# Kernel optimization log

Measured on AMD Instinct MI355X. Metric: run time of the kernel, lower is better.

## Reference

```python
import jax, jax.numpy as jnp
import numpy as np

SCALE_WEIGHT = 0.5 ** 0.5
B, C, T, S = 8, 512, 2048, 2048


def setup_inputs() -> dict:
    key = jax.random.key(0)
    ks = jax.random.split(key, 6)
    return {
        "base_target_emb": jax.random.normal(ks[0], (B, C, T, 1), dtype=jnp.float32),
        "input_from_dec": jax.random.normal(ks[1], (B, C, T, 1), dtype=jnp.float32),
        "encoder_out_top": jax.random.normal(ks[2], (B, C, S), dtype=jnp.float32),
        "encoder_out_combine": jax.random.normal(ks[3], (B, C, S), dtype=jnp.float32),
        "W": jax.random.normal(ks[4], (C, C), dtype=jnp.float32) * (1.0 / np.sqrt(C)),
        "b": jax.random.normal(ks[5], (C,), dtype=jnp.float32) * 0.01,
    }


def reference(base_target_emb, input_from_dec, encoder_out_top, encoder_out_combine, W, b):
    # seq_linear: per-token Linear over the channel dim. torch Linear: h = x @ W.T + b, W is [out,in]
    x = input_from_dec[..., 0]                                # [B,C,T]
    preatt = jnp.einsum('oc,bct->bot', W, x) + b[None, :, None]  # [B,C,T]
    target = (base_target_emb[..., 0] + preatt) * SCALE_WEIGHT   # [B,C,T]
    pre_attn = jnp.einsum('bct,bcs->bts', target, encoder_out_top)  # [B,T,S]
    attn = jax.nn.softmax(pre_attn, axis=2)                      # [B,T,S]
    ctx = jnp.einsum('bts,bcs->btc', attn, encoder_out_combine)  # [B,T,C]
    context_output = jnp.transpose(ctx, (0, 2, 1))[..., None]    # [B,C,T,1]
    return context_output, attn
```

## Files before the change

### kernel.cpp

```cpp
#include <hip/hip_runtime.h>
#include <cstddef>
#include <cstdint>

#define SCALE_WEIGHT 0.70710678118654752440f

static constexpr int B_ = 8, C_ = 512, T_ = 2048, S_ = 2048;
static constexpr size_t BCT_ = (size_t)B_ * C_ * T_;
static constexpr size_t BTS_ = (size_t)B_ * T_ * S_;

typedef _Float16 half_t;
typedef half_t half8  __attribute__((ext_vector_type(8)));
typedef half_t half4v __attribute__((ext_vector_type(4)));
typedef float  floatx4 __attribute__((ext_vector_type(4)));

__device__ __forceinline__ void gload_lds16(const void* g, void* l) {
    __builtin_amdgcn_global_load_lds(
        (const __attribute__((address_space(1))) void*)g,
        (__attribute__((address_space(3))) void*)l, 16, 0, 0);
}

__global__ __launch_bounds__(256) void transpose_cvt_kernel(
    const float* __restrict__ in, half_t* __restrict__ out, int R, int Cc)
{
    __shared__ float tile[64][65];
    const int b  = blockIdx.z;
    const int r0 = blockIdx.y * 64, c0 = blockIdx.x * 64;
    const float* ib = in + (size_t)b * R * Cc;
    half_t* ob = out + (size_t)b * R * Cc;
    const int t  = threadIdx.x;
    const int rr = t >> 4, cq = t & 15;
    #pragma unroll
    for (int i = 0; i < 4; ++i) {
        const int r = rr + i * 16;
        float4 v = *(const float4*)&ib[(size_t)(r0 + r) * Cc + c0 + cq * 4];
        tile[cq * 4 + 0][r] = v.x;
        tile[cq * 4 + 1][r] = v.y;
        tile[cq * 4 + 2][r] = v.z;
        tile[cq * 4 + 3][r] = v.w;
    }
    __syncthreads();
    const int cw = t >> 4, rq = (t & 15) * 4;
    #pragma unroll
    for (int i = 0; i < 4; ++i) {
        const int c = cw + i * 16;
        half4v h = {(half_t)tile[c][rq + 0], (half_t)tile[c][rq + 1],
                    (half_t)tile[c][rq + 2], (half_t)tile[c][rq + 3]};
        *(half4v*)&ob[(size_t)(c0 + c) * R + r0 + rq] = h;
    }
}

__global__ __launch_bounds__(256) void cvt_f32_f16_kernel(
    const float* __restrict__ in, half_t* __restrict__ out, int n4)
{
    const int stride = gridDim.x * blockDim.x;
    for (int i = blockIdx.x * blockDim.x + threadIdx.x; i < n4; i += stride) {
        float4 v = ((const float4*)in)[i];
        half4v h = {(half_t)v.x, (half_t)v.y, (half_t)v.z, (half_t)v.w};
        ((half4v*)out)[i] = h;
    }
}

template<int EPI>
__global__ __launch_bounds__(256) void gemm_f16_db_kernel(
    const half_t* __restrict__ A, const half_t* __restrict__ Bm,
    float* __restrict__ Cout, half_t* __restrict__ CoutH,
    const float* __restrict__ base, const float* __restrict__ bias,
    int M, int N, int K, size_t sA, size_t sB, size_t sC)
{
    __shared__ __align__(128) half_t As[2][128 * 64];
    __shared__ __align__(128) half_t Bs[2][128 * 64];

    const int tid  = threadIdx.x;
    const int lane = tid & 63, w = tid >> 6;
    const int wr = w >> 1, wc = w & 1;
    const int b  = blockIdx.z;
    const int m0 = blockIdx.y * 128, n0 = blockIdx.x * 128;

    const half_t* Ab = A  + (size_t)b * sA;
    const half_t* Bb = Bm + (size_t)b * sB;

    const int lr = lane >> 3;
    const int sw = (lane & 7) ^ lr;
    const half_t* aG[4]; const half_t* bG[4];
    int dOff[4];
    #pragma unroll
    for (int i = 0; i < 4; ++i) {
        const int r = w * 32 + i * 8 + lr;
        aG[i] = Ab + (size_t)(m0 + r) * K + sw * 8;
        bG[i] = Bb + (size_t)(n0 + r) * K + sw * 8;
        dOff[i] = (w * 32 + i * 8) * 128;
    }

    const int fr = lane & 15, kg = lane >> 4;
    int aoff[4], boff[4];
    #pragma unroll
    for (int mi = 0; mi < 4; ++mi) {
        const int m = wr * 64 + mi * 16 + fr;
        aoff[mi] = m * 128 + ((kg ^ (m & 7)) << 4);
    }
    #pragma unroll
    for (int nj = 0; nj < 4; ++nj) {
        const int n = wc * 64 + nj * 16 + fr;
        boff[nj] = n * 128 + ((kg ^ (n & 7)) << 4);
    }

    floatx4 acc[4][4];
    #pragma unroll
    for (int mi = 0; mi < 4; ++mi)
        #pragma unroll
        for (int nj = 0; nj < 4; ++nj)
            acc[mi][nj] = (floatx4){0.f, 0.f, 0.f, 0.f};

    auto STAGE = [&](int t, int pg) {
        const int k0 = t * 64;
        char* Ad = (char*)As[pg];
        char* Bd = (char*)Bs[pg];
        #pragma unroll
        for (int i = 0; i < 4; ++i) {
            gload_lds16(aG[i] + k0, Ad + dOff[i]);
            gload_lds16(bG[i] + k0, Bd + dOff[i]);
        }
    };

    auto COMPUTE = [&](int pg) {
        const char* Ar = (const char*)As[pg];
        const char* Br = (const char*)Bs[pg];
        #pragma unroll
        for (int kk = 0; kk < 2; ++kk) {
            half8 af[4], bf[4];
            #pragma unroll
            for (int mi = 0; mi < 4; ++mi)
                af[mi] = *(const half8*)(Ar + (aoff[mi] ^ (kk << 6)));
            #pragma unroll
            for (int nj = 0; nj < 4; ++nj)
                bf[nj] = *(const half8*)(Br + (boff[nj] ^ (kk << 6)));
            #pragma unroll
            for (int mi = 0; mi < 4; ++mi)
                #pragma unroll
                for (int nj = 0; nj < 4; ++nj)
                    acc[mi][nj] = __builtin_amdgcn_mfma_f32_16x16x32_f16(
                        af[mi], bf[nj], acc[mi][nj], 0, 0, 0);
        }
    };

    const int NT = K >> 6;
    STAGE(0, 0);
    int cur = 0;
    for (int t = 0; t < NT - 1; ++t) {
        STAGE(t + 1, cur ^ 1);
        asm volatile("s_waitcnt vmcnt(8)" ::: "memory");
        __builtin_amdgcn_s_barrier();
        __builtin_amdgcn_sched_barrier(0);
        COMPUTE(cur);
        asm volatile("s_waitcnt lgkmcnt(0)" ::: "memory");
        __builtin_amdgcn_sched_barrier(0);
        __builtin_amdgcn_s_barrier();
        __builtin_amdgcn_sched_barrier(0);
        cur ^= 1;
    }
    asm volatile("s_waitcnt vmcnt(0)" ::: "memory");
    __builtin_amdgcn_s_barrier();
    __builtin_amdgcn_sched_barrier(0);
    COMPUTE(cur);

    if constexpr (EPI == 0) {
        float* Cb = Cout + (size_t)b * sC;
        #pragma unroll
        for (int mi = 0; mi < 4; ++mi) {
            const int row = m0 + wr * 64 + mi * 16 + (lane >> 4) * 4;
            #pragma unroll
            for (int nj = 0; nj < 4; ++nj) {
                const int col = n0 + wc * 64 + nj * 16 + (lane & 15);
                #pragma unroll
                for (int r = 0; r < 4; ++r)
                    Cb[(size_t)(row + r) * N + col] = acc[mi][nj][r];
            }
        }
    } else {
        half_t* Cb = CoutH + (size_t)b * sC;
        #pragma unroll
        for (int nj = 0; nj < 4; ++nj) {
            const int col = n0 + wc * 64 + nj * 16 + (lane & 15);
            const float bn = bias[col];
            const float* bp = base + ((size_t)b * N + col) * (size_t)M;
            #pragma unroll
            for (int mi = 0; mi < 4; ++mi) {
                const int row = m0 + wr * 64 + mi * 16 + (lane >> 4) * 4;
                #pragma unroll
                for (int r = 0; r < 4; ++r) {
                    float v = (acc[mi][nj][r] + bn + bp[row + r]) * SCALE_WEIGHT;
                    Cb[(size_t)(row + r) * N + col] = (half_t)v;
                }
            }
        }
    }
}

__global__ __launch_bounds__(256) void k3_softmax_kernel(
    float* __restrict__ logits, half_t* __restrict__ attnh)
{
    float* p = logits + (size_t)blockIdx.x * S_;
    half4v* ph = (half4v*)(attnh + (size_t)blockIdx.x * S_);
    const int tid = threadIdx.x;
    float4 v0 = *(const float4*)&p[tid * 4];
    float4 v1 = *(const float4*)&p[tid * 4 + 1024];

    float mx = fmaxf(fmaxf(fmaxf(v0.x, v0.y), fmaxf(v0.z, v0.w)),
                     fmaxf(fmaxf(v1.x, v1.y), fmaxf(v1.z, v1.w)));
    #pragma unroll
    for (int off = 32; off; off >>= 1)
        mx = fmaxf(mx, __shfl_xor(mx, off));

    __shared__ float sm[4];
    __shared__ float ss[4];
    const int wid = tid >> 6, lane = tid & 63;
    if (lane == 0) sm[wid] = mx;
    __syncthreads();
    const float rmax = fmaxf(fmaxf(sm[0], sm[1]), fmaxf(sm[2], sm[3]));

    float e[8];
    e[0] = __expf(v0.x - rmax); e[1] = __expf(v0.y - rmax);
    e[2] = __expf(v0.z - rmax); e[3] = __expf(v0.w - rmax);
    e[4] = __expf(v1.x - rmax); e[5] = __expf(v1.y - rmax);
    e[6] = __expf(v1.z - rmax); e[7] = __expf(v1.w - rmax);

    float sum = 0.f;
    #pragma unroll
    for (int i = 0; i < 8; ++i) sum += e[i];
    #pragma unroll
    for (int off = 32; off; off >>= 1)
        sum += __shfl_xor(sum, off);
    if (lane == 0) ss[wid] = sum;
    __syncthreads();
    const float inv = 1.f / (ss[0] + ss[1] + ss[2] + ss[3]);

    float4 r0, r1;
    r0.x = e[0] * inv; r0.y = e[1] * inv; r0.z = e[2] * inv; r0.w = e[3] * inv;
    r1.x = e[4] * inv; r1.y = e[5] * inv; r1.z = e[6] * inv; r1.w = e[7] * inv;
    *(float4*)&p[tid * 4] = r0;
    *(float4*)&p[tid * 4 + 1024] = r1;
    ph[tid]       = (half4v){(half_t)r0.x, (half_t)r0.y, (half_t)r0.z, (half_t)r0.w};
    ph[tid + 256] = (half4v){(half_t)r1.x, (half_t)r1.y, (half_t)r1.z, (half_t)r1.w};
}

extern "C" void kernel_launch(void* const* d_in, const int* in_sizes, int n_in,
                              void* d_out, int out_size, void* d_ws, size_t ws_size,
                              hipStream_t stream) {
    const float* base = (const float*)d_in[0];
    const float* x    = (const float*)d_in[1];
    const float* top  = (const float*)d_in[2];
    const float* comb = (const float*)d_in[3];
    const float* W    = (const float*)d_in[4];
    const float* bias = (const float*)d_in[5];

    float* out    = (float*)d_out;
    float* ctx    = out;
    float* logits = out + BCT_;

    half_t* xT   = (half_t*)d_out;
    half_t* topT = xT + BCT_;

    half_t* attnh = (half_t*)d_ws;
    half_t* tgtT  = attnh;
    half_t* combh = attnh + BTS_;
    half_t* Wh    = combh + (size_t)B_ * C_ * S_;

    transpose_cvt_kernel<<<dim3(T_ / 64, C_ / 64, B_), 256, 0, stream>>>(x, xT, C_, T_);
    transpose_cvt_kernel<<<dim3(S_ / 64, C_ / 64, B_), 256, 0, stream>>>(top, topT, C_, S_);
    cvt_f32_f16_kernel<<<2048, 256, 0, stream>>>(comb, combh, (int)((size_t)B_ * C_ * S_ / 4));
    cvt_f32_f16_kernel<<<256, 256, 0, stream>>>(W, Wh, C_ * C_ / 4);

    gemm_f16_db_kernel<1><<<dim3(C_ / 128, T_ / 128, B_), 256, 0, stream>>>(
        xT, Wh, nullptr, tgtT, base, bias,
        T_, C_, C_, (size_t)T_ * C_, 0, (size_t)T_ * C_);

    gemm_f16_db_kernel<0><<<dim3(S_ / 128, T_ / 128, B_), 256, 0, stream>>>(
        tgtT, topT, logits, nullptr, nullptr, nullptr,
        T_, S_, C_, (size_t)T_ * C_, (size_t)S_ * C_, (size_t)T_ * S_);

    k3_softmax_kernel<<<dim3(B_ * T_), 256, 0, stream>>>(logits, attnh);

    gemm_f16_db_kernel<0><<<dim3(T_ / 128, C_ / 128, B_), 256, 0, stream>>>(
        combh, attnh, ctx, nullptr, nullptr, nullptr,
        C_, T_, S_, (size_t)C_ * S_, (size_t)T_ * S_, (size_t)C_ * T_);
}
```

Baseline: 212.0 us.

## Fuse logits GEMM with online softmax into one kernel

Replaces the QK^T GEMM plus separate softmax kernel with a fused kernel. Each 512-thread block computes 64 rows across all of S, tracks an online running max and sum, and stores unnormalized fp16 exponentials to a workspace. It then rescales them into the fp32 attn output and the fp16 copy. This removes the fp32 logits write and re-read, at the cost of a 64-row tile per block and only 256 blocks, which may underuse the GPU, plus an extra fp16 workspace round trip.

```diff
diff --git a/kernel.cpp b/kernel.cpp
--- a/kernel.cpp
+++ b/kernel.cpp
@@ -196,51 +196,199 @@
     }
 }
 
-__global__ __launch_bounds__(256) void k3_softmax_kernel(
-    float* __restrict__ logits, half_t* __restrict__ attnh)
+__global__ __launch_bounds__(512) void k23_fused_kernel(
+    const half_t* __restrict__ tgtT, const half_t* __restrict__ topT,
+    float* __restrict__ attnf, half_t* __restrict__ attnh,
+    half_t* __restrict__ pws)
 {
-    float* p = logits + (size_t)blockIdx.x * S_;
-    half4v* ph = (half4v*)(attnh + (size_t)blockIdx.x * S_);
-    const int tid = threadIdx.x;
-    float4 v0 = *(const float4*)&p[tid * 4];
-    float4 v1 = *(const float4*)&p[tid * 4 + 1024];
-
-    float mx = fmaxf(fmaxf(fmaxf(v0.x, v0.y), fmaxf(v0.z, v0.w)),
-                     fmaxf(fmaxf(v1.x, v1.y), fmaxf(v1.z, v1.w)));
-    #pragma unroll
-    for (int off = 32; off; off >>= 1)
-        mx = fmaxf(mx, __shfl_xor(mx, off));
-
-    __shared__ float sm[4];
-    __shared__ float ss[4];
-    const int wid = tid >> 6, lane = tid & 63;
-    if (lane == 0) sm[wid] = mx;
+    __shared__ __align__(128) half_t Atile[64 * 512];
+    __shared__ __align__(128) half_t Bbuf[2][128 * 64];
+    __shared__ __align__(128) half_t ptile[64 * 128];
+    __shared__ float mu[16 * 64];
+    __shared__ float msh[64], ssh[64];
+    __shared__ float pmax[4][64], psum[4][64];
+
+    const int tid = threadIdx.x, lane = tid & 63, w = tid >> 6;
+    const int wr = w >> 2, wc = w & 3;
+    const int b = blockIdx.x, tt = blockIdx.y;
+    const int fr = lane & 15, kg = lane >> 4;
+    const int q4 = (lane >> 4) << 2;
+
+    const half_t* Ab = tgtT + ((size_t)(b * T_ + tt * 64)) * C_;
+    const half_t* Bb = topT + (size_t)b * S_ * C_;
+    half_t* pblk = pws + ((size_t)(b * 32 + tt)) * 64 * 2048;
+
+    if (tid < 64) { msh[tid] = -3.0e38f; ssh[tid] = 0.f; }
+
+    #pragma unroll
+    for (int i = 0; i < 8; ++i) {
+        const int row = w * 8 + i;
+        gload_lds16(Ab + (size_t)row * C_ + ((lane ^ (row & 7)) << 3),
+                    (char*)Atile + row * 1024);
+    }
+
+    auto STAGE_B = [&](int q, int pg) {
+        const int s0 = (q >> 3) * 128, k0 = (q & 7) * 64;
+        char* dst = (char*)Bbuf[pg];
+        #pragma unroll
+        for (int j = 0; j < 2; ++j) {
+            const int r8 = w * 16 + j * 8;
+            gload_lds16(Bb + (size_t)(s0 + r8 + (lane >> 3)) * C_ + k0 +
+                            (((lane & 7) ^ (lane >> 3)) << 3),
+                        dst + r8 * 128);
+        }
+    };
+
+    STAGE_B(0, 0);
+    int buf = 0;
+
+    for (int st = 0; st < 16; ++st) {
+        floatx4 acc[2][2];
+        #pragma unroll
+        for (int mi = 0; mi < 2; ++mi)
+            #pragma unroll
+            for (int nj = 0; nj < 2; ++nj)
+                acc[mi][nj] = (floatx4){0.f, 0.f, 0.f, 0.f};
+
+        for (int kc = 0; kc < 8; ++kc) {
+            const int q = st * 8 + kc;
+            if (q < 127) {
+                STAGE_B(q + 1, buf ^ 1);
+                asm volatile("s_waitcnt vmcnt(2)" ::: "memory");
+            } else {
+                asm volatile("s_waitcnt vmcnt(0)" ::: "memory");
+            }
+            __builtin_amdgcn_s_barrier();
+            __builtin_amdgcn_sched_barrier(0);
+
+            const char* Ar = (const char*)Atile;
+            const char* Br = (const char*)Bbuf[buf];
+            #pragma unroll
+            for (int kk = 0; kk < 2; ++kk) {
+                half8 af[2], bf[2];
+                #pragma unroll
+                for (int mi = 0; mi < 2; ++mi) {
+                    const int m = wr * 32 + mi * 16 + fr;
+                    af[mi] = *(const half8*)(Ar + m * 1024 +
+                              (((kc * 8 + kk * 4 + kg) ^ (m & 7)) << 4));
+                }
+                #pragma unroll
+                for (int nj = 0; nj < 2; ++nj) {
+                    const int n = wc * 32 + nj * 16 + fr;
+                    bf[nj] = *(const half8*)(Br + n * 128 +
+                              (((kk * 4 + kg) ^ (n & 7)) << 4));
+                }
+                #pragma unroll
+                for (int mi = 0; mi < 2; ++mi)
+                    #pragma unroll
+                    for (int nj = 0; nj < 2; ++nj)
+                        acc[mi][nj] = __builtin_amdgcn_mfma_f32_16x16x32_f16(
+                            af[mi], bf[nj], acc[mi][nj], 0, 0, 0);
+            }
+
+            asm volatile("s_waitcnt lgkmcnt(0)" ::: "memory");
+            __builtin_amdgcn_sched_barrier(0);
+            __builtin_amdgcn_s_barrier();
+            __builtin_amdgcn_sched_barrier(0);
+            buf ^= 1;
+        }
+
+        #pragma unroll
+        for (int mi = 0; mi < 2; ++mi)
+            #pragma unroll
+            for (int r = 0; r < 4; ++r) {
+                float v = fmaxf(acc[mi][0][r], acc[mi][1][r]);
+                v = fmaxf(v, __shfl_xor(v, 1));
+                v = fmaxf(v, __shfl_xor(v, 2));
+                v = fmaxf(v, __shfl_xor(v, 4));
+                v = fmaxf(v, __shfl_xor(v, 8));
+                if (fr == 0) pmax[wc][wr * 32 + mi * 16 + q4 + r] = v;
+            }
+        __syncthreads();
+
+        float scaleReg = 0.f;
+        if (tid < 64) {
+            float tm = fmaxf(fmaxf(pmax[0][tid], pmax[1][tid]),
+                             fmaxf(pmax[2][tid], pmax[3][tid]));
+            float mo = msh[tid];
+            float mn = fmaxf(mo, tm);
+            msh[tid] = mn;
+            mu[st * 64 + tid] = mn;
+            scaleReg = __expf(mo - mn);
+        }
+        __syncthreads();
+
+        #pragma unroll
+        for (int mi = 0; mi < 2; ++mi)
+            #pragma unroll
+            for (int r = 0; r < 4; ++r) {
+                const int row = wr * 32 + mi * 16 + q4 + r;
+                const float mn = msh[row];
+                float p0 = __expf(acc[mi][0][r] - mn);
+                float p1 = __expf(acc[mi][1][r] - mn);
+                ptile[row * 128 + wc * 32 + fr]      = (half_t)p0;
+                ptile[row * 128 + wc * 32 + 16 + fr] = (half_t)p1;
+                float s = p0 + p1;
+                s += __shfl_xor(s, 1);
+                s += __shfl_xor(s, 2);
+                s += __shfl_xor(s, 4);
+                s += __shfl_xor(s, 8);
+                if (fr == 0) psum[wc][row] = s;
+            }
+        __syncthreads();
+
+        if (tid < 64)
+            ssh[tid] = ssh[tid] * scaleReg +
+                       psum[0][tid] + psum[1][tid] + psum[2][tid] + psum[3][tid];
+
+        {
+            const int row = tid >> 3, cg = (tid & 7) * 16;
+            half8 v0 = *(const half8*)&ptile[row * 128 + cg];
+            half8 v1 = *(const half8*)&ptile[row * 128 + cg + 8];
+            *(half8*)&pblk[(size_t)row * 2048 + st * 128 + cg]     = v0;
+            *(half8*)&pblk[(size_t)row * 2048 + st * 128 + cg + 8] = v1;
+        }
+    }
+
     __syncthreads();
-    const float rmax = fmaxf(fmaxf(sm[0], sm[1]), fmaxf(sm[2], sm[3]));
-
-    float e[8];
-    e[0] = __expf(v0.x - rmax); e[1] = __expf(v0.y - rmax);
-    e[2] = __expf(v0.z - rmax); e[3] = __expf(v0.w - rmax);
-    e[4] = __expf(v1.x - rmax); e[5] = __expf(v1.y - rmax);
-    e[6] = __expf(v1.z - rmax); e[7] = __expf(v1.w - rmax);
-
-    float sum = 0.f;
-    #pragma unroll
-    for (int i = 0; i < 8; ++i) sum += e[i];
-    #pragma unroll
-    for (int off = 32; off; off >>= 1)
-        sum += __shfl_xor(sum, off);
-    if (lane == 0) ss[wid] = sum;
+    for (int i = tid; i < 1024; i += 512) {
+        const int row = i & 63;
+        mu[i] = __expf(mu[i] - msh[row]) / ssh[row];
+    }
     __syncthreads();
-    const float inv = 1.f / (ss[0] + ss[1] + ss[2] + ss[3]);
-
-    float4 r0, r1;
-    r0.x = e[0] * inv; r0.y = e[1] * inv; r0.z = e[2] * inv; r0.w = e[3] * inv;
-    r1.x = e[4] * inv; r1.y = e[5] * inv; r1.z = e[6] * inv; r1.w = e[7] * inv;
-    *(float4*)&p[tid * 4] = r0;
-    *(float4*)&p[tid * 4 + 1024] = r1;
-    ph[tid]       = (half4v){(half_t)r0.x, (half_t)r0.y, (half_t)r0.z, (half_t)r0.w};
-    ph[tid + 256] = (half4v){(half_t)r1.x, (half_t)r1.y, (half_t)r1.z, (half_t)r1.w};
+
+    #pragma unroll 1
+    for (int it = 0; it < 16; ++it) {
+        const int e = (it * 512 + tid) * 16;
+        const int row = e >> 11, col = e & 2047;
+        const float f = mu[(col >> 7) * 64 + row];
+        half8 v0 = *(const half8*)&pblk[(size_t)row * 2048 + col];
+        half8 v1 = *(const half8*)&pblk[(size_t)row * 2048 + col + 8];
+        const size_t oidx = ((size_t)(b * T_ + tt * 64 + row)) * S_ + col;
+        float4 o; half8 h0, h1;
+        float a0 = (float)v0[0] * f, a1 = (float)v0[1] * f;
+        float a2 = (float)v0[2] * f, a3 = (float)v0[3] * f;
+        o = (float4){a0, a1, a2, a3};
+        *(float4*)&attnf[oidx] = o;
+        h0[0] = (half_t)a0; h0[1] = (half_t)a1; h0[2] = (half_t)a2; h0[3] = (half_t)a3;
+        a0 = (float)v0[4] * f; a1 = (float)v0[5] * f;
+        a2 = (float)v0[6] * f; a3 = (float)v0[7] * f;
+        o = (float4){a0, a1, a2, a3};
+        *(float4*)&attnf[oidx + 4] = o;
+        h0[4] = (half_t)a0; h0[5] = (half_t)a1; h0[6] = (half_t)a2; h0[7] = (half_t)a3;
+        a0 = (float)v1[0] * f; a1 = (float)v1[1] * f;
+        a2 = (float)v1[2] * f; a3 = (float)v1[3] * f;
+        o = (float4){a0, a1, a2, a3};
+        *(float4*)&attnf[oidx + 8] = o;
+        h1[0] = (half_t)a0; h1[1] = (half_t)a1; h1[2] = (half_t)a2; h1[3] = (half_t)a3;
+        a0 = (float)v1[4] * f; a1 = (float)v1[5] * f;
+        a2 = (float)v1[6] * f; a3 = (float)v1[7] * f;
+        o = (float4){a0, a1, a2, a3};
+        *(float4*)&attnf[oidx + 12] = o;
+        h1[4] = (half_t)a0; h1[5] = (half_t)a1; h1[6] = (half_t)a2; h1[7] = (half_t)a3;
+        *(half8*)&attnh[oidx]     = h0;
+        *(half8*)&attnh[oidx + 8] = h1;
+    }
 }
 
 extern "C" void kernel_launch(void* const* d_in, const int* in_sizes, int n_in,
@@ -253,17 +401,18 @@
     const float* W    = (const float*)d_in[4];
     const float* bias = (const float*)d_in[5];
 
-    float* out    = (float*)d_out;
-    float* ctx    = out;
-    float* logits = out + BCT_;
+    float* out   = (float*)d_out;
+    float* ctx   = out;
+    float* attnf = out + BCT_;
 
     half_t* xT   = (half_t*)d_out;
     half_t* topT = xT + BCT_;
 
-    half_t* attnh = (half_t*)d_ws;
-    half_t* tgtT  = attnh;
+    half_t* pws   = (half_t*)d_ws;
+    half_t* attnh = pws + (size_t)256 * 64 * 2048;
     half_t* combh = attnh + BTS_;
     half_t* Wh    = combh + (size_t)B_ * C_ * S_;
+    half_t* tgtT  = Wh + (size_t)C_ * C_;
 
     transpose_cvt_kernel<<<dim3(T_ / 64, C_ / 64, B_), 256, 0, stream>>>(x, xT, C_, T_);
     transpose_cvt_kernel<<<dim3(S_ / 64, C_ / 64, B_), 256, 0, stream>>>(top, topT, C_, S_);
@@ -274,11 +423,8 @@
         xT, Wh, nullptr, tgtT, base, bias,
         T_, C_, C_, (size_t)T_ * C_, 0, (size_t)T_ * C_);
 
-    gemm_f16_db_kernel<0><<<dim3(S_ / 128, T_ / 128, B_), 256, 0, stream>>>(
-        tgtT, topT, logits, nullptr, nullptr, nullptr,
-        T_, S_, C_, (size_t)T_ * C_, (size_t)S_ * C_, (size_t)T_ * S_);
-
-    k3_softmax_kernel<<<dim3(B_ * T_), 256, 0, stream>>>(logits, attnh);
+    k23_fused_kernel<<<dim3(B_, T_ / 64), 512, 0, stream>>>(
+        tgtT, topT, attnf, attnh, pws);
 
     gemm_f16_db_kernel<0><<<dim3(T_ / 128, C_ / 128, B_), 256, 0, stream>>>(
         combh, attnh, ctx, nullptr, nullptr, nullptr,
```

Result: slower. 330.1 us (+55.7%).

## Fuse partial softmax into logits GEMM epilogue and merge prep kernels

Applied to the files above, without the earlier changes.

The logits GEMM now computes per-tile row maxima and exp-sums in its epilogue and writes unnormalized fp16 probabilities plus per-tile max/sum arrays. A lighter second pass combines the 16 partial statistics per row and rescales to produce the fp32 attention output and the fp16 copy. This removes the fp32 logits write and read round trip. The transpose and conversion launches are also merged pairwise to cut launch count. It adds fp16 rounding of unnormalized exponentials before rescaling, which may shift precision slightly.

```diff
diff --git a/kernel.cpp b/kernel.cpp
--- a/kernel.cpp
+++ b/kernel.cpp
@@ -19,20 +19,24 @@
         (__attribute__((address_space(3))) void*)l, 16, 0, 0);
 }
 
-__global__ __launch_bounds__(256) void transpose_cvt_kernel(
-    const float* __restrict__ in, half_t* __restrict__ out, int R, int Cc)
+__global__ __launch_bounds__(256) void transpose2_cvt_kernel(
+    const float* __restrict__ x, const float* __restrict__ top,
+    half_t* __restrict__ xT, half_t* __restrict__ topT)
 {
     __shared__ float tile[64][65];
-    const int b  = blockIdx.z;
+    const int z = blockIdx.z;
+    const float* in = (z < 8) ? x : top;
+    half_t* outp = (z < 8) ? xT : topT;
+    const int b  = z & 7;
     const int r0 = blockIdx.y * 64, c0 = blockIdx.x * 64;
-    const float* ib = in + (size_t)b * R * Cc;
-    half_t* ob = out + (size_t)b * R * Cc;
+    const float* ib = in + (size_t)b * C_ * T_;
+    half_t* ob = outp + (size_t)b * C_ * T_;
     const int t  = threadIdx.x;
     const int rr = t >> 4, cq = t & 15;
     #pragma unroll
     for (int i = 0; i < 4; ++i) {
         const int r = rr + i * 16;
-        float4 v = *(const float4*)&ib[(size_t)(r0 + r) * Cc + c0 + cq * 4];
+        float4 v = *(const float4*)&ib[(size_t)(r0 + r) * T_ + c0 + cq * 4];
         tile[cq * 4 + 0][r] = v.x;
         tile[cq * 4 + 1][r] = v.y;
         tile[cq * 4 + 2][r] = v.z;
@@ -45,18 +49,22 @@
         const int c = cw + i * 16;
         half4v h = {(half_t)tile[c][rq + 0], (half_t)tile[c][rq + 1],
                     (half_t)tile[c][rq + 2], (half_t)tile[c][rq + 3]};
-        *(half4v*)&ob[(size_t)(c0 + c) * R + r0 + rq] = h;
-    }
-}
-
-__global__ __launch_bounds__(256) void cvt_f32_f16_kernel(
-    const float* __restrict__ in, half_t* __restrict__ out, int n4)
+        *(half4v*)&ob[(size_t)(c0 + c) * C_ + r0 + rq] = h;
+    }
+}
+
+__global__ __launch_bounds__(256) void cvt2_f32_f16_kernel(
+    const float* __restrict__ comb, half_t* __restrict__ combh,
+    const float* __restrict__ W, half_t* __restrict__ Wh,
+    int n4a, int n4tot)
 {
     const int stride = gridDim.x * blockDim.x;
-    for (int i = blockIdx.x * blockDim.x + threadIdx.x; i < n4; i += stride) {
-        float4 v = ((const float4*)in)[i];
-        half4v h = {(half_t)v.x, (half_t)v.y, (half_t)v.z, (half_t)v.w};
-        ((half4v*)out)[i] = h;
+    for (int i = blockIdx.x * blockDim.x + threadIdx.x; i < n4tot; i += stride) {
+        const float4* src; half4v* dst; int j;
+        if (i < n4a) { src = (const float4*)comb; dst = (half4v*)combh; j = i; }
+        else         { src = (const float4*)W;    dst = (half4v*)Wh;    j = i - n4a; }
+        float4 v = src[j];
+        dst[j] = (half4v){(half_t)v.x, (half_t)v.y, (half_t)v.z, (half_t)v.w};
     }
 }
 
@@ -196,51 +204,190 @@
     }
 }
 
-__global__ __launch_bounds__(256) void k3_softmax_kernel(
-    float* __restrict__ logits, half_t* __restrict__ attnh)
+__global__ __launch_bounds__(256) void k2p_kernel(
+    const half_t* __restrict__ A, const half_t* __restrict__ Bm,
+    half_t* __restrict__ P, float* __restrict__ mArr, float* __restrict__ sArr)
 {
-    float* p = logits + (size_t)blockIdx.x * S_;
-    half4v* ph = (half4v*)(attnh + (size_t)blockIdx.x * S_);
+    __shared__ __align__(128) half_t As[2][128 * 64];
+    __shared__ __align__(128) half_t Bs[2][128 * 64];
+    __shared__ float rmax[2][128];
+    __shared__ float rsum[2][128];
+
+    const int tid  = threadIdx.x;
+    const int lane = tid & 63, w = tid >> 6;
+    const int wr = w >> 1, wc = w & 1;
+    const int b  = blockIdx.z;
+    const int m0 = blockIdx.y * 128, n0 = blockIdx.x * 128;
+    constexpr int K = C_;
+
+    const half_t* Ab = A  + (size_t)b * T_ * C_;
+    const half_t* Bb = Bm + (size_t)b * S_ * C_;
+
+    const int lr = lane >> 3;
+    const int sw = (lane & 7) ^ lr;
+    const half_t* aG[4]; const half_t* bG[4];
+    int dOff[4];
+    #pragma unroll
+    for (int i = 0; i < 4; ++i) {
+        const int r = w * 32 + i * 8 + lr;
+        aG[i] = Ab + (size_t)(m0 + r) * K + sw * 8;
+        bG[i] = Bb + (size_t)(n0 + r) * K + sw * 8;
+        dOff[i] = (w * 32 + i * 8) * 128;
+    }
+
+    const int fr = lane & 15, kg = lane >> 4;
+    const int q4 = kg * 4;
+    int aoff[4], boff[4];
+    #pragma unroll
+    for (int mi = 0; mi < 4; ++mi) {
+        const int m = wr * 64 + mi * 16 + fr;
+        aoff[mi] = m * 128 + ((kg ^ (m & 7)) << 4);
+    }
+    #pragma unroll
+    for (int nj = 0; nj < 4; ++nj) {
+        const int n = wc * 64 + nj * 16 + fr;
+        boff[nj] = n * 128 + ((kg ^ (n & 7)) << 4);
+    }
+
+    floatx4 acc[4][4];
+    #pragma unroll
+    for (int mi = 0; mi < 4; ++mi)
+        #pragma unroll
+        for (int nj = 0; nj < 4; ++nj)
+            acc[mi][nj] = (floatx4){0.f, 0.f, 0.f, 0.f};
+
+    auto STAGE = [&](int t, int pg) {
+        const int k0 = t * 64;
+        char* Ad = (char*)As[pg];
+        char* Bd = (char*)Bs[pg];
+        #pragma unroll
+        for (int i = 0; i < 4; ++i) {
+            gload_lds16(aG[i] + k0, Ad + dOff[i]);
+            gload_lds16(bG[i] + k0, Bd + dOff[i]);
+        }
+    };
+
+    auto COMPUTE = [&](int pg) {
+        const char* Ar = (const char*)As[pg];
+        const char* Br = (const char*)Bs[pg];
+        #pragma unroll
+        for (int kk = 0; kk < 2; ++kk) {
+            half8 af[4], bf[4];
+            #pragma unroll
+            for (int mi = 0; mi < 4; ++mi)
+                af[mi] = *(const half8*)(Ar + (aoff[mi] ^ (kk << 6)));
+            #pragma unroll
+            for (int nj = 0; nj < 4; ++nj)
+                bf[nj] = *(const half8*)(Br + (boff[nj] ^ (kk << 6)));
+            #pragma unroll
+            for (int mi = 0; mi < 4; ++mi)
+                #pragma unroll
+                for (int nj = 0; nj < 4; ++nj)
+                    acc[mi][nj] = __builtin_amdgcn_mfma_f32_16x16x32_f16(
+                        af[mi], bf[nj], acc[mi][nj], 0, 0, 0);
+        }
+    };
+
+    constexpr int NT = K >> 6;
+    STAGE(0, 0);
+    int cur = 0;
+    for (int t = 0; t < NT - 1; ++t) {
+        STAGE(t + 1, cur ^ 1);
+        asm volatile("s_waitcnt vmcnt(8)" ::: "memory");
+        __builtin_amdgcn_s_barrier();
+        __builtin_amdgcn_sched_barrier(0);
+        COMPUTE(cur);
+        asm volatile("s_waitcnt lgkmcnt(0)" ::: "memory");
+        __builtin_amdgcn_sched_barrier(0);
+        __builtin_amdgcn_s_barrier();
+        __builtin_amdgcn_sched_barrier(0);
+        cur ^= 1;
+    }
+    asm volatile("s_waitcnt vmcnt(0)" ::: "memory");
+    __builtin_amdgcn_s_barrier();
+    __builtin_amdgcn_sched_barrier(0);
+    COMPUTE(cur);
+
+    #pragma unroll
+    for (int mi = 0; mi < 4; ++mi) {
+        #pragma unroll
+        for (int r = 0; r < 4; ++r) {
+            float v = fmaxf(fmaxf(acc[mi][0][r], acc[mi][1][r]),
+                            fmaxf(acc[mi][2][r], acc[mi][3][r]));
+            v = fmaxf(v, __shfl_xor(v, 1));
+            v = fmaxf(v, __shfl_xor(v, 2));
+            v = fmaxf(v, __shfl_xor(v, 4));
+            v = fmaxf(v, __shfl_xor(v, 8));
+            if (fr == 0) rmax[wc][wr * 64 + mi * 16 + q4 + r] = v;
+        }
+    }
+    __syncthreads();
+
+    half_t* Pb = P + ((size_t)(b * T_ + m0)) * S_;
+    #pragma unroll
+    for (int mi = 0; mi < 4; ++mi) {
+        #pragma unroll
+        for (int r = 0; r < 4; ++r) {
+            const int row = wr * 64 + mi * 16 + q4 + r;
+            const float mC = fmaxf(rmax[0][row], rmax[1][row]);
+            float s = 0.f;
+            #pragma unroll
+            for (int nj = 0; nj < 4; ++nj) {
+                float pv = __expf(acc[mi][nj][r] - mC);
+                s += pv;
+                Pb[(size_t)row * S_ + n0 + wc * 64 + nj * 16 + fr] = (half_t)pv;
+            }
+            s += __shfl_xor(s, 1);
+            s += __shfl_xor(s, 2);
+            s += __shfl_xor(s, 4);
+            s += __shfl_xor(s, 8);
+            if (fr == 0) rsum[wc][row] = s;
+        }
+    }
+    __syncthreads();
+
+    if (tid < 128) {
+        const float m = fmaxf(rmax[0][tid], rmax[1][tid]);
+        const float s = rsum[0][tid] + rsum[1][tid];
+        const size_t si = ((size_t)(b * 16 + (n0 >> 7))) * T_ + m0 + tid;
+        mArr[si] = m;
+        sArr[si] = s;
+    }
+}
+
+__global__ __launch_bounds__(256) void k3b_kernel(
+    const half_t* __restrict__ P, const float* __restrict__ mArr,
+    const float* __restrict__ sArr, float* __restrict__ attnf,
+    half_t* __restrict__ attnh)
+{
+    const int bid = blockIdx.x;
+    const int b = bid >> 11, t = bid & 2047;
     const int tid = threadIdx.x;
-    float4 v0 = *(const float4*)&p[tid * 4];
-    float4 v1 = *(const float4*)&p[tid * 4 + 1024];
-
-    float mx = fmaxf(fmaxf(fmaxf(v0.x, v0.y), fmaxf(v0.z, v0.w)),
-                     fmaxf(fmaxf(v1.x, v1.y), fmaxf(v1.z, v1.w)));
-    #pragma unroll
-    for (int off = 32; off; off >>= 1)
-        mx = fmaxf(mx, __shfl_xor(mx, off));
-
-    __shared__ float sm[4];
-    __shared__ float ss[4];
-    const int wid = tid >> 6, lane = tid & 63;
-    if (lane == 0) sm[wid] = mx;
-    __syncthreads();
-    const float rmax = fmaxf(fmaxf(sm[0], sm[1]), fmaxf(sm[2], sm[3]));
-
-    float e[8];
-    e[0] = __expf(v0.x - rmax); e[1] = __expf(v0.y - rmax);
-    e[2] = __expf(v0.z - rmax); e[3] = __expf(v0.w - rmax);
-    e[4] = __expf(v1.x - rmax); e[5] = __expf(v1.y - rmax);
-    e[6] = __expf(v1.z - rmax); e[7] = __expf(v1.w - rmax);
-
-    float sum = 0.f;
-    #pragma unroll
-    for (int i = 0; i < 8; ++i) sum += e[i];
-    #pragma unroll
-    for (int off = 32; off; off >>= 1)
-        sum += __shfl_xor(sum, off);
-    if (lane == 0) ss[wid] = sum;
-    __syncthreads();
-    const float inv = 1.f / (ss[0] + ss[1] + ss[2] + ss[3]);
-
-    float4 r0, r1;
-    r0.x = e[0] * inv; r0.y = e[1] * inv; r0.z = e[2] * inv; r0.w = e[3] * inv;
-    r1.x = e[4] * inv; r1.y = e[5] * inv; r1.z = e[6] * inv; r1.w = e[7] * inv;
-    *(float4*)&p[tid * 4] = r0;
-    *(float4*)&p[tid * 4 + 1024] = r1;
-    ph[tid]       = (half4v){(half_t)r0.x, (half_t)r0.y, (half_t)r0.z, (half_t)r0.w};
-    ph[tid + 256] = (half4v){(half_t)r1.x, (half_t)r1.y, (half_t)r1.z, (half_t)r1.w};
+
+    float mfin = -3.0e38f;
+    #pragma unroll
+    for (int j = 0; j < 16; ++j)
+        mfin = fmaxf(mfin, mArr[((size_t)(b * 16 + j)) * T_ + t]);
+    float sig = 0.f;
+    #pragma unroll
+    for (int j = 0; j < 16; ++j)
+        sig += sArr[((size_t)(b * 16 + j)) * T_ + t] *
+               __expf(mArr[((size_t)(b * 16 + j)) * T_ + t] - mfin);
+    const float inv = 1.f / sig;
+    const float f = __expf(mArr[((size_t)(b * 16 + (tid >> 4))) * T_ + t] - mfin) * inv;
+
+    const size_t rb = (size_t)bid * S_ + tid * 8;
+    half8 v = *(const half8*)&P[rb];
+    float a0 = (float)v[0] * f, a1 = (float)v[1] * f;
+    float a2 = (float)v[2] * f, a3 = (float)v[3] * f;
+    float a4 = (float)v[4] * f, a5 = (float)v[5] * f;
+    float a6 = (float)v[6] * f, a7 = (float)v[7] * f;
+    *(float4*)&attnf[rb]     = (float4){a0, a1, a2, a3};
+    *(float4*)&attnf[rb + 4] = (float4){a4, a5, a6, a7};
+    half8 h;
+    h[0] = (half_t)a0; h[1] = (half_t)a1; h[2] = (half_t)a2; h[3] = (half_t)a3;
+    h[4] = (half_t)a4; h[5] = (half_t)a5; h[6] = (half_t)a6; h[7] = (half_t)a7;
+    *(half8*)&attnh[rb] = h;
 }
 
 extern "C" void kernel_launch(void* const* d_in, const int* in_sizes, int n_in,
@@ -253,32 +400,36 @@
     const float* W    = (const float*)d_in[4];
     const float* bias = (const float*)d_in[5];
 
-    float* out    = (float*)d_out;
-    float* ctx    = out;
-    float* logits = out + BCT_;
+    float* out   = (float*)d_out;
+    float* ctx   = out;
+    float* attnf = out + BCT_;
 
     half_t* xT   = (half_t*)d_out;
     half_t* topT = xT + BCT_;
 
-    half_t* attnh = (half_t*)d_ws;
-    half_t* tgtT  = attnh;
+    half_t* pws   = (half_t*)d_ws;
+    half_t* attnh = pws + BTS_;
     half_t* combh = attnh + BTS_;
     half_t* Wh    = combh + (size_t)B_ * C_ * S_;
-
-    transpose_cvt_kernel<<<dim3(T_ / 64, C_ / 64, B_), 256, 0, stream>>>(x, xT, C_, T_);
-    transpose_cvt_kernel<<<dim3(S_ / 64, C_ / 64, B_), 256, 0, stream>>>(top, topT, C_, S_);
-    cvt_f32_f16_kernel<<<2048, 256, 0, stream>>>(comb, combh, (int)((size_t)B_ * C_ * S_ / 4));
-    cvt_f32_f16_kernel<<<256, 256, 0, stream>>>(W, Wh, C_ * C_ / 4);
+    half_t* tgtT  = Wh + (size_t)C_ * C_;
+    float*  mArr  = (float*)(tgtT + BCT_);
+    float*  sArr  = mArr + (size_t)B_ * 16 * T_;
+
+    transpose2_cvt_kernel<<<dim3(T_ / 64, C_ / 64, 16), 256, 0, stream>>>(x, top, xT, topT);
+    {
+        const int n4a = (int)((size_t)B_ * C_ * S_ / 4);
+        const int n4tot = n4a + C_ * C_ / 4;
+        cvt2_f32_f16_kernel<<<2048, 256, 0, stream>>>(comb, combh, W, Wh, n4a, n4tot);
+    }
 
     gemm_f16_db_kernel<1><<<dim3(C_ / 128, T_ / 128, B_), 256, 0, stream>>>(
         xT, Wh, nullptr, tgtT, base, bias,
         T_, C_, C_, (size_t)T_ * C_, 0, (size_t)T_ * C_);
 
-    gemm_f16_db_kernel<0><<<dim3(S_ / 128, T_ / 128, B_), 256, 0, stream>>>(
-        tgtT, topT, logits, nullptr, nullptr, nullptr,
-        T_, S_, C_, (size_t)T_ * C_, (size_t)S_ * C_, (size_t)T_ * S_);
-
-    k3_softmax_kernel<<<dim3(B_ * T_), 256, 0, stream>>>(logits, attnh);
+    k2p_kernel<<<dim3(S_ / 128, T_ / 128, B_), 256, 0, stream>>>(
+        tgtT, topT, pws, mArr, sArr);
+
+    k3b_kernel<<<dim3(B_ * T_), 256, 0, stream>>>(pws, mArr, sArr, attnf, attnh);
 
     gemm_f16_db_kernel<0><<<dim3(T_ / 128, C_ / 128, B_), 256, 0, stream>>>(
         combh, attnh, ctx, nullptr, nullptr, nullptr,
```

After: 261.3 us. +23.3%, slower.
